# Kernel optimization log

Hardware: AMD Instinct MI355X
Metric: run time of the kernel (lower is better)

## Reference

```python
import jax, jax.numpy as jnp
import numpy as np
import math

D_MODEL = 2048
NUM_HEADS = 32
NUM_KV_HEADS = 8
HEAD_DIM = D_MODEL // NUM_HEADS  # 64
BATCH = 2
SEQ = 2048


def setup_inputs() -> dict:
    key = jax.random.key(0)
    ks = jax.random.split(key, 5)
    std_q = math.sqrt(2.0 / (D_MODEL + D_MODEL))
    std_kv = math.sqrt(2.0 / (D_MODEL + NUM_KV_HEADS * HEAD_DIM))
    x = jax.random.normal(ks[0], (BATCH, SEQ, D_MODEL), dtype=jnp.float32)
    Wq = jax.random.normal(ks[1], (D_MODEL, D_MODEL), dtype=jnp.float32) * std_q
    Wk = jax.random.normal(ks[2], (NUM_KV_HEADS * HEAD_DIM, D_MODEL), dtype=jnp.float32) * std_kv
    Wv = jax.random.normal(ks[3], (NUM_KV_HEADS * HEAD_DIM, D_MODEL), dtype=jnp.float32) * std_kv
    Wo = jax.random.normal(ks[4], (D_MODEL, D_MODEL), dtype=jnp.float32) * std_q
    return {"x": x, "Wq": Wq, "Wk": Wk, "Wv": Wv, "Wo": Wo}


def reference(x, Wq, Wk, Wv, Wo):
    B, L, _ = x.shape
    group = NUM_HEADS // NUM_KV_HEADS
    # projections: x @ W.T
    q = (x @ Wq.T).reshape(B, L, NUM_HEADS, HEAD_DIM).transpose(0, 2, 1, 3)      # [B,H,L,D]
    k = (x @ Wk.T).reshape(B, L, NUM_KV_HEADS, HEAD_DIM).transpose(0, 2, 1, 3)   # [B,Hkv,L,D]
    v = (x @ Wv.T).reshape(B, L, NUM_KV_HEADS, HEAD_DIM).transpose(0, 2, 1, 3)
    # expand KV heads (repeat_interleave along head dim)
    k = jnp.repeat(k, group, axis=1)  # [B,H,L,D]
    v = jnp.repeat(v, group, axis=1)
    scale = 1.0 / math.sqrt(HEAD_DIM)
    scores = jnp.einsum("bhld,bhsd->bhls", q, k) * scale  # [B,H,L,S]
    causal_mask = jnp.tril(jnp.ones((L, L), dtype=bool))
    scores = jnp.where(causal_mask[None, None], scores, -jnp.inf)
    weights = jax.nn.softmax(scores, axis=-1)
    out = jnp.einsum("bhls,bhsd->bhld", weights, v)  # [B,H,L,D]
    out = out.transpose(0, 2, 1, 3).reshape(B, L, D_MODEL)
    return out @ Wo.T
```

## Files before the change

kernel.cpp:

```cpp
#include <hip/hip_runtime.h>
#include <stdint.h>


typedef unsigned short u16;
typedef short bf16x8 __attribute__((ext_vector_type(8)));
typedef float f32x4 __attribute__((ext_vector_type(4)));

#define D_MODEL 2048
#define QKV_DIM 3072
#define NUM_HEADS 32
#define HEAD_DIM 64
#define SEQ 2048
#define MTOT 4096

static __device__ __forceinline__ u16 f2bf(float f){
  uint32_t u = __builtin_bit_cast(uint32_t, f);
  u += 0x7FFFu + ((u >> 16) & 1u);
  return (u16)(u >> 16);
}

static __device__ __forceinline__ float exp2_fast(float x){
  float r;
  asm("v_exp_f32 %0, %1" : "=v"(r) : "v"(x));
  return r;
}

static __device__ __forceinline__ uint32_t cvt_pk_bf16(float lo, float hi){
  uint32_t r;
  asm("v_cvt_pk_bf16_f32 %0, %1, %2" : "=v"(r) : "v"(lo), "v"(hi));
  return r;
}

static __device__ __forceinline__ void gload16(const u16* g, u16* l){
  __builtin_amdgcn_global_load_lds(
      (__attribute__((address_space(1))) uint32_t*)(uintptr_t)g,
      (__attribute__((address_space(3))) uint32_t*)l,
      16, 0, 0);
}

__global__ __launch_bounds__(256)
void cvt_bf16(const float* __restrict__ in, u16* __restrict__ out, int n,
              float scl){
  const int i = (blockIdx.x * 256 + threadIdx.x) * 8;
  if (i >= n) return;
  float4 a = *(const float4*)(in + i);
  float4 b = *(const float4*)(in + i + 4);
  union { u16 h[8]; uint4 v; } t;
  t.h[0]=f2bf(a.x*scl); t.h[1]=f2bf(a.y*scl); t.h[2]=f2bf(a.z*scl); t.h[3]=f2bf(a.w*scl);
  t.h[4]=f2bf(b.x*scl); t.h[5]=f2bf(b.y*scl); t.h[6]=f2bf(b.z*scl); t.h[7]=f2bf(b.w*scl);
  *(uint4*)(out + i) = t.v;
}

template <bool F32OUT>
__global__ __launch_bounds__(256)
void gemm_bt(const u16* __restrict__ A, const u16* __restrict__ B,
             void* __restrict__ Cv, int M, int N, int K){
  constexpr int BK = 32;
  __shared__ __attribute__((aligned(16))) u16 As[128*BK];
  __shared__ __attribute__((aligned(16))) u16 Bs[128*BK];
  const int tid  = threadIdx.x;
  const int wave = tid >> 6, lane = tid & 63;
  const int quad = lane >> 4, l16 = lane & 15;
  const int wrow = wave >> 1, wcol = wave & 1;
  const int m0 = blockIdx.y * 128, n0 = blockIdx.x * 128;
  const int srow = lane >> 2, scol = (lane & 3) * 8;

  const f32x4 zero = {0.f, 0.f, 0.f, 0.f};
  f32x4 acc[4][4];
#pragma unroll
  for (int i = 0; i < 4; i++)
#pragma unroll
    for (int j = 0; j < 4; j++) acc[i][j] = zero;

  for (int k0 = 0; k0 < K; k0 += BK){
#pragma unroll
    for (int t = 0; t < 2; t++){
      const int chunk = wave + t*4;
      gload16(A + (size_t)(m0 + chunk*16 + srow)*K + k0 + scol, As + chunk*16*BK);
      gload16(B + (size_t)(n0 + chunk*16 + srow)*K + k0 + scol, Bs + chunk*16*BK);
    }
    __syncthreads();
    bf16x8 af[4], bfr[4];
#pragma unroll
    for (int mi = 0; mi < 4; mi++)
      af[mi] = *(const bf16x8*)(As + (wrow*64 + mi*16 + l16)*BK + quad*8);
#pragma unroll
    for (int ni = 0; ni < 4; ni++)
      bfr[ni] = *(const bf16x8*)(Bs + (wcol*64 + ni*16 + l16)*BK + quad*8);
#pragma unroll
    for (int mi = 0; mi < 4; mi++)
#pragma unroll
      for (int ni = 0; ni < 4; ni++)
        acc[mi][ni] = __builtin_amdgcn_mfma_f32_16x16x32_bf16(af[mi], bfr[ni], acc[mi][ni], 0, 0, 0);
    __syncthreads();
  }
#pragma unroll
  for (int mi = 0; mi < 4; mi++)
#pragma unroll
    for (int ni = 0; ni < 4; ni++){
      const int col = n0 + wcol*64 + ni*16 + l16;
#pragma unroll
      for (int r = 0; r < 4; r++){
        const int row = m0 + wrow*64 + mi*16 + quad*4 + r;
        if constexpr (F32OUT)
          ((float*)Cv)[(size_t)row*N + col] = acc[mi][ni][r];
        else
          ((u16*)Cv)[(size_t)row*N + col] = f2bf(acc[mi][ni][r]);
      }
    }
}

__global__ __launch_bounds__(256)
void vtrans(const u16* __restrict__ QKV, u16* __restrict__ VT){
  __shared__ u16 Ls[64*72];
  const int tid = threadIdx.x;
  const int st = blockIdx.x, hk = blockIdx.y, b = blockIdx.z;
  const size_t rb = (size_t)b * SEQ;
#pragma unroll
  for (int t = 0; t < 2; t++){
    const int task = t*256 + tid;
    const int r = task >> 3, c = task & 7;
    *(uint4*)(Ls + r*72 + c*8) =
        *(const uint4*)(QKV + (rb + st*64 + r)*QKV_DIM + 2560 + hk*HEAD_DIM + c*8);
  }
  __syncthreads();
  u16* vt_g = VT + ((size_t)(b*8 + hk) * 64) * SEQ;
#pragma unroll
  for (int t = 0; t < 2; t++){
    const int task = t*256 + tid;
    const int d = task >> 3, sc = task & 7;
    union { u16 h[8]; uint4 v; } tmp;
#pragma unroll
    for (int e = 0; e < 8; e++){
      const int key = ((2*(sc>>2) + (e>>2))<<4) + ((sc&3)<<2) + (e&3);
      tmp.h[e] = Ls[key*72 + d];
    }
    *(uint4*)(vt_g + (size_t)d*SEQ + st*64 + sc*8) = tmp.v;
  }
}

__global__ __launch_bounds__(256)
void attn(const u16* __restrict__ Q, const u16* __restrict__ Kp,
          const u16* __restrict__ VT, u16* __restrict__ O, int qs, int ks){
  constexpr int KP = 72;
  __shared__ __attribute__((aligned(16))) u16 Ks[64*KP];
  __shared__ __attribute__((aligned(16))) u16 Vt[64*KP];
  const int tid = threadIdx.x;
  const int wave = tid >> 6, lane = tid & 63, quad = lane >> 4, l16 = lane & 15;
  const int g_ = (blockIdx.x + blockIdx.y) & 31;
  const int qt = blockIdx.z ? (31 - g_) : g_;
  const int h = blockIdx.y, b = blockIdx.z;
  const int hk = h >> 2;
  const size_t rb = (size_t)b * SEQ;
  const u16* vt_g = VT + ((size_t)(b*8 + hk) * 64) * SEQ;

  const int sr = tid >> 2, sc = tid & 3;
  const int qrow = wave*16 + l16;

  bf16x8 qf[2];
  {
    const u16* qp = Q + (rb + qt*64 + wave*16 + l16)*qs + h*HEAD_DIM;
    qf[0] = *(const bf16x8*)(qp + quad*8);
    qf[1] = *(const bf16x8*)(qp + 32 + quad*8);
  }
  const f32x4 zero = {0.f, 0.f, 0.f, 0.f};
  f32x4 oacc[4];
#pragma unroll
  for (int i = 0; i < 4; i++) oacc[i] = zero;
  float m_i = -INFINITY;
  float l_i = 0.f;

  const u16* kg_base = Kp + (rb + sr)*ks + hk*HEAD_DIM;
  const u16* vg_base = vt_g + (size_t)sr*SEQ;

  for (int j = 0; j <= qt; ++j){
    {
      const u16* kg = kg_base + (size_t)(j*64)*ks;
      const u16* vg = vg_base + j*64;
      uint4 k0 = *(const uint4*)(kg + sc*8);
      uint4 k1 = *(const uint4*)(kg + (sc+4)*8);
      uint4 v0 = *(const uint4*)(vg + sc*8);
      uint4 v1 = *(const uint4*)(vg + (sc+4)*8);
      *(uint4*)(Ks + sr*KP + sc*8)     = k0;
      *(uint4*)(Ks + sr*KP + (sc+4)*8) = k1;
      *(uint4*)(Vt + sr*KP + sc*8)     = v0;
      *(uint4*)(Vt + sr*KP + (sc+4)*8) = v1;
    }
    __syncthreads();

    f32x4 st[4];
#pragma unroll
    for (int ni = 0; ni < 4; ni++){
      f32x4 s = zero;
#pragma unroll
      for (int ss = 0; ss < 2; ss++){
        bf16x8 kf = *(const bf16x8*)(Ks + (ni*16 + l16)*KP + ss*32 + quad*8);
        s = __builtin_amdgcn_mfma_f32_16x16x32_bf16(kf, qf[ss], s, 0, 0, 0);
      }
      st[ni] = s;
    }
    if (j == qt){
#pragma unroll
      for (int ni = 0; ni < 4; ni++)
#pragma unroll
        for (int r = 0; r < 4; r++)
          if (ni*16 + quad*4 + r > qrow) st[ni][r] = -INFINITY;
    }

    float mx = fmaxf(fmaxf(fmaxf(st[0][0], st[0][1]), fmaxf(st[0][2], st[0][3])),
                     fmaxf(fmaxf(st[1][0], st[1][1]), fmaxf(st[1][2], st[1][3])));
    mx = fmaxf(mx, fmaxf(fmaxf(fmaxf(st[2][0], st[2][1]), fmaxf(st[2][2], st[2][3])),
                         fmaxf(fmaxf(st[3][0], st[3][1]), fmaxf(st[3][2], st[3][3]))));
    mx = fmaxf(mx, __shfl_xor(mx, 16));
    mx = fmaxf(mx, __shfl_xor(mx, 32));

    if (__all(mx <= m_i + 10.f)){
      float ps = 0.f;
#pragma unroll
      for (int ni = 0; ni < 4; ni++)
#pragma unroll
        for (int r = 0; r < 4; r++){
          const float p = exp2_fast(st[ni][r] - m_i);
          st[ni][r] = p;
          ps += p;
        }
      ps += __shfl_xor(ps, 16);
      ps += __shfl_xor(ps, 32);
      l_i += ps;
    } else {
      const float mn = fmaxf(m_i, mx);
      const float alpha = exp2_fast(m_i - mn);
      float ps = 0.f;
#pragma unroll
      for (int ni = 0; ni < 4; ni++)
#pragma unroll
        for (int r = 0; r < 4; r++){
          const float p = exp2_fast(st[ni][r] - mn);
          st[ni][r] = p;
          ps += p;
        }
      ps += __shfl_xor(ps, 16);
      ps += __shfl_xor(ps, 32);
      l_i = l_i*alpha + ps;
      m_i = mn;
      float ar[4];
#pragma unroll
      for (int r = 0; r < 4; r++) ar[r] = __shfl(alpha, quad*4 + r);
#pragma unroll
      for (int ci = 0; ci < 4; ci++)
#pragma unroll
        for (int r = 0; r < 4; r++) oacc[ci][r] *= ar[r];
    }

    bf16x8 pfr[2];
#pragma unroll
    for (int ss = 0; ss < 2; ss++){
      union { uint32_t w[4]; bf16x8 v; } pk;
      pk.w[0] = cvt_pk_bf16(st[2*ss][0],   st[2*ss][1]);
      pk.w[1] = cvt_pk_bf16(st[2*ss][2],   st[2*ss][3]);
      pk.w[2] = cvt_pk_bf16(st[2*ss+1][0], st[2*ss+1][1]);
      pk.w[3] = cvt_pk_bf16(st[2*ss+1][2], st[2*ss+1][3]);
      pfr[ss] = pk.v;
    }

#pragma unroll
    for (int ss = 0; ss < 2; ss++)
#pragma unroll
      for (int ci = 0; ci < 4; ci++){
        bf16x8 vf = *(const bf16x8*)(Vt + (ci*16 + l16)*KP + ss*32 + quad*8);
        oacc[ci] = __builtin_amdgcn_mfma_f32_16x16x32_bf16(pfr[ss], vf, oacc[ci], 0, 0, 0);
      }
    __syncthreads();
  }

  float lf[4];
#pragma unroll
  for (int r = 0; r < 4; r++) lf[r] = __shfl(l_i, quad*4 + r);
#pragma unroll
  for (int ci = 0; ci < 4; ci++)
#pragma unroll
    for (int r = 0; r < 4; r++){
      const size_t row = rb + qt*64 + wave*16 + quad*4 + r;
      O[row*D_MODEL + h*HEAD_DIM + ci*16 + l16] = f2bf(oacc[ci][r] / lf[r]);
    }
}

extern "C" void kernel_launch(void* const* d_in, const int* in_sizes, int n_in,
                              void* d_out, int out_size, void* d_ws, size_t ws_size,
                              hipStream_t stream){
  const float* x  = (const float*)d_in[0];
  const float* Wq = (const float*)d_in[1];
  const float* Wk = (const float*)d_in[2];
  const float* Wv = (const float*)d_in[3];
  const float* Wo = (const float*)d_in[4];
  float* out = (float*)d_out;

  u16* xb   = (u16*)d_ws;
  u16* Wb   = xb + (size_t)MTOT*D_MODEL;
  u16* VTb  = Wb + (size_t)QKV_DIM*D_MODEL;
  u16* QKVb = (u16*)d_out;

  const int nx  = MTOT*D_MODEL;
  const int nwq = D_MODEL*D_MODEL;
  const int nwk = 512*D_MODEL;
  const float QSCL = 0.125f * 1.44269504f;

  cvt_bf16<<<nx/2048, 256, 0, stream>>>(x, xb, nx, 1.0f);
  cvt_bf16<<<nwq/2048, 256, 0, stream>>>(Wq, Wb, nwq, QSCL);
  cvt_bf16<<<nwk/2048, 256, 0, stream>>>(Wk, Wb + (size_t)D_MODEL*D_MODEL, nwk, 1.0f);
  cvt_bf16<<<nwk/2048, 256, 0, stream>>>(Wv, Wb + (size_t)2560*D_MODEL, nwk, 1.0f);
  gemm_bt<false><<<dim3(QKV_DIM/128, MTOT/128), 256, 0, stream>>>(xb, Wb, QKVb, MTOT, QKV_DIM, D_MODEL);
  vtrans<<<dim3(SEQ/64, 8, 2), 256, 0, stream>>>(QKVb, VTb);
  attn<<<dim3(SEQ/64, NUM_HEADS, 2), 256, 0, stream>>>(
      QKVb, QKVb + D_MODEL, VTb, xb, QKV_DIM, QKV_DIM);
  cvt_bf16<<<nwq/2048, 256, 0, stream>>>(Wo, Wb, nwq, 1.0f);
  gemm_bt<true><<<dim3(D_MODEL/128, MTOT/128), 256, 0, stream>>>(xb, Wb, (void*)out, MTOT, D_MODEL, D_MODEL);
}
```

Baseline: 346.7 us.

## Pre-tile and XOR-swizzle K/V into contiguous tiles, load via direct-to-LDS

```diff
diff --git a/kernel.cpp b/kernel.cpp
--- a/kernel.cpp
+++ b/kernel.cpp
@@ -111,11 +111,21 @@
 }
 
 __global__ __launch_bounds__(256)
-void vtrans(const u16* __restrict__ QKV, u16* __restrict__ VT){
+void kvtrans(const u16* __restrict__ QKV, u16* __restrict__ Ksw,
+             u16* __restrict__ Vsw){
   __shared__ u16 Ls[64*72];
   const int tid = threadIdx.x;
   const int st = blockIdx.x, hk = blockIdx.y, b = blockIdx.z;
   const size_t rb = (size_t)b * SEQ;
+  const size_t tbase = ((size_t)(b*8 + hk)*32 + st) * 4096;
+
+#pragma unroll
+  for (int t = 0; t < 2; t++){
+    const int task = t*256 + tid;
+    const int r = task >> 3, c = task & 7;
+    uint4 kv = *(const uint4*)(QKV + (rb + st*64 + r)*QKV_DIM + 2048 + hk*HEAD_DIM + c*8);
+    *(uint4*)(Ksw + tbase + r*64 + (size_t)((c ^ (r & 7)) * 8)) = kv;
+  }
 #pragma unroll
   for (int t = 0; t < 2; t++){
     const int task = t*256 + tid;
@@ -124,7 +134,6 @@
         *(const uint4*)(QKV + (rb + st*64 + r)*QKV_DIM + 2560 + hk*HEAD_DIM + c*8);
   }
   __syncthreads();
-  u16* vt_g = VT + ((size_t)(b*8 + hk) * 64) * SEQ;
 #pragma unroll
   for (int t = 0; t < 2; t++){
     const int task = t*256 + tid;
@@ -135,16 +144,15 @@
       const int key = ((2*(sc>>2) + (e>>2))<<4) + ((sc&3)<<2) + (e&3);
       tmp.h[e] = Ls[key*72 + d];
     }
-    *(uint4*)(vt_g + (size_t)d*SEQ + st*64 + sc*8) = tmp.v;
+    *(uint4*)(Vsw + tbase + d*64 + (size_t)((sc ^ (d & 7)) * 8)) = tmp.v;
   }
 }
 
 __global__ __launch_bounds__(256)
-void attn(const u16* __restrict__ Q, const u16* __restrict__ Kp,
-          const u16* __restrict__ VT, u16* __restrict__ O, int qs, int ks){
-  constexpr int KP = 72;
-  __shared__ __attribute__((aligned(16))) u16 Ks[64*KP];
-  __shared__ __attribute__((aligned(16))) u16 Vt[64*KP];
+void attn(const u16* __restrict__ Q, const u16* __restrict__ Ksw,
+          const u16* __restrict__ Vsw, u16* __restrict__ O, int qs){
+  __shared__ __attribute__((aligned(16))) u16 Ks[64*64];
+  __shared__ __attribute__((aligned(16))) u16 Vt[64*64];
   const int tid = threadIdx.x;
   const int wave = tid >> 6, lane = tid & 63, quad = lane >> 4, l16 = lane & 15;
   const int g_ = (blockIdx.x + blockIdx.y) & 31;
@@ -152,10 +160,10 @@
   const int h = blockIdx.y, b = blockIdx.z;
   const int hk = h >> 2;
   const size_t rb = (size_t)b * SEQ;
-  const u16* vt_g = VT + ((size_t)(b*8 + hk) * 64) * SEQ;
-
-  const int sr = tid >> 2, sc = tid & 3;
+  const size_t hb = ((size_t)(b*8 + hk)) * 32;
+
   const int qrow = wave*16 + l16;
+  const int sw = l16 & 7;
 
   bf16x8 qf[2];
   {
@@ -170,21 +178,16 @@
   float m_i = -INFINITY;
   float l_i = 0.f;
 
-  const u16* kg_base = Kp + (rb + sr)*ks + hk*HEAD_DIM;
-  const u16* vg_base = vt_g + (size_t)sr*SEQ;
-
   for (int j = 0; j <= qt; ++j){
     {
-      const u16* kg = kg_base + (size_t)(j*64)*ks;
-      const u16* vg = vg_base + j*64;
-      uint4 k0 = *(const uint4*)(kg + sc*8);
-      uint4 k1 = *(const uint4*)(kg + (sc+4)*8);
-      uint4 v0 = *(const uint4*)(vg + sc*8);
-      uint4 v1 = *(const uint4*)(vg + (sc+4)*8);
-      *(uint4*)(Ks + sr*KP + sc*8)     = k0;
-      *(uint4*)(Ks + sr*KP + (sc+4)*8) = k1;
-      *(uint4*)(Vt + sr*KP + sc*8)     = v0;
-      *(uint4*)(Vt + sr*KP + (sc+4)*8) = v1;
+      const u16* kt = Ksw + (hb + j) * 4096;
+      const u16* vt = Vsw + (hb + j) * 4096;
+#pragma unroll
+      for (int t = 0; t < 2; t++){
+        const int ch = wave*2 + t;
+        gload16(kt + ch*512 + lane*8, Ks + ch*512);
+        gload16(vt + ch*512 + lane*8, Vt + ch*512);
+      }
     }
     __syncthreads();
 
@@ -194,7 +197,8 @@
       f32x4 s = zero;
 #pragma unroll
       for (int ss = 0; ss < 2; ss++){
-        bf16x8 kf = *(const bf16x8*)(Ks + (ni*16 + l16)*KP + ss*32 + quad*8);
+        bf16x8 kf = *(const bf16x8*)(Ks + ((ni*16 + l16) << 6) +
+                                     (((ss*4 + quad) ^ sw) << 3));
         s = __builtin_amdgcn_mfma_f32_16x16x32_bf16(kf, qf[ss], s, 0, 0, 0);
       }
       st[ni] = s;
@@ -267,7 +271,8 @@
     for (int ss = 0; ss < 2; ss++)
 #pragma unroll
       for (int ci = 0; ci < 4; ci++){
-        bf16x8 vf = *(const bf16x8*)(Vt + (ci*16 + l16)*KP + ss*32 + quad*8);
+        bf16x8 vf = *(const bf16x8*)(Vt + ((ci*16 + l16) << 6) +
+                                     (((ss*4 + quad) ^ sw) << 3));
         oacc[ci] = __builtin_amdgcn_mfma_f32_16x16x32_bf16(pfr[ss], vf, oacc[ci], 0, 0, 0);
       }
     __syncthreads();
@@ -297,8 +302,9 @@
 
   u16* xb   = (u16*)d_ws;
   u16* Wb   = xb + (size_t)MTOT*D_MODEL;
-  u16* VTb  = Wb + (size_t)QKV_DIM*D_MODEL;
   u16* QKVb = (u16*)d_out;
+  u16* Kswz = Wb;
+  u16* Vswz = Wb + (size_t)2*1024*1024;
 
   const int nx  = MTOT*D_MODEL;
   const int nwq = D_MODEL*D_MODEL;
@@ -310,9 +316,9 @@
   cvt_bf16<<<nwk/2048, 256, 0, stream>>>(Wk, Wb + (size_t)D_MODEL*D_MODEL, nwk, 1.0f);
   cvt_bf16<<<nwk/2048, 256, 0, stream>>>(Wv, Wb + (size_t)2560*D_MODEL, nwk, 1.0f);
   gemm_bt<false><<<dim3(QKV_DIM/128, MTOT/128), 256, 0, stream>>>(xb, Wb, QKVb, MTOT, QKV_DIM, D_MODEL);
-  vtrans<<<dim3(SEQ/64, 8, 2), 256, 0, stream>>>(QKVb, VTb);
+  kvtrans<<<dim3(SEQ/64, 8, 2), 256, 0, stream>>>(QKVb, Kswz, Vswz);
   attn<<<dim3(SEQ/64, NUM_HEADS, 2), 256, 0, stream>>>(
-      QKVb, QKVb + D_MODEL, VTb, xb, QKV_DIM, QKV_DIM);
+      QKVb, Kswz, Vswz, xb, QKV_DIM);
   cvt_bf16<<<nwq/2048, 256, 0, stream>>>(Wo, Wb, nwq, 1.0f);
   gemm_bt<true><<<dim3(D_MODEL/128, MTOT/128), 256, 0, stream>>>(xb, Wb, (void*)out, MTOT, D_MODEL, D_MODEL);
 }
```

After: 343.2 us. About the same (-1.0%).
